# Kernel tuning notes

Measured on AMD Instinct MI355X. Metric: run time of the kernel, lower is better.

## Reference

```python
import jax, jax.numpy as jnp
import numpy as np

B, T, CIN, CH, M, NCLS = 2048, 8, 2048, 1024, 32, 21
EPS = 1e-8  # torch.cosine_similarity eps


def setup_inputs() -> dict:
    key = jax.random.key(0)
    ks = jax.random.split(key, 16)
    g = lambda k, shp, sc=0.02: jax.random.normal(k, shp, dtype=jnp.float32) * sc
    return {
        "x": g(ks[0], (B, T, CIN), 1.0),
        "static_feat": g(ks[1], (NCLS, CIN, M), 1.0),  # 21 kmeans exemplar banks
        "Wk": g(ks[2], (CH, CIN)), "bk": g(ks[3], (CH,)),
        "Wv": g(ks[4], (CH, CIN)), "bv": g(ks[5], (CH,)),
        "WEk": g(ks[6], (CH, CIN)), "bEk": g(ks[7], (CH,)),
        "WEv": g(ks[8], (CH, CIN)), "bEv": g(ks[9], (CH,)),
        "Ww": g(ks[10], (1, CH)), "bw": g(ks[11], (1,)),
        "Wout": g(ks[12], (NCLS, 2 * CH)), "bout": g(ks[13], (NCLS,)),
    }


def reference(x, static_feat, Wk, bk, Wv, bv, WEk, bEk, WEv, bEv, Ww, bw, Wout, bout):
    # last frame only: [B, CIN]
    xl = x[:, -1, :]
    # 1x1 convs on length-1 sequence == dense projections
    k = xl @ Wk.T + bk          # [B, CH]
    v = xl @ Wv.T + bv          # [B, CH]
    # project all 21 static memories at once: [NCLS, CH, M]
    Ek = jnp.einsum('oc,ncm->nom', WEk, static_feat) + bEk[None, :, None]
    Ev = jnp.einsum('oc,ncm->nom', WEv, static_feat) + bEv[None, :, None]
    # cosine similarity along channel dim (torch clamps each norm at eps)
    kn = k / jnp.maximum(jnp.linalg.norm(k, axis=1, keepdims=True), EPS)
    Ekn = Ek / jnp.maximum(jnp.linalg.norm(Ek, axis=1, keepdims=True), EPS)
    cos = jnp.einsum('bo,nom->bnm', kn, Ekn)      # [B, NCLS, M]
    w = jax.nn.softmax(cos, axis=-1)               # softmax over exemplars
    s = jnp.einsum('nom,bnm->bno', Ev, w)          # weighted sums [B, NCLS, CH]
    # per-class scalar weights via conv2_1_W, softmax over the 21 classes
    fw = jax.nn.softmax(s @ Ww[0] + bw[0], axis=-1)  # [B, NCLS]
    fE = jnp.einsum('bno,bn->bo', s, fw)             # [B, CH]
    h = jax.nn.relu(jnp.concatenate([v, fE], axis=-1))  # [B, 2*CH]
    out = h @ Wout.T + bout                              # [B, NCLS]
    return out[:, :, None]  # [B, NCLS, 1] to match Conv1d output
```

## Files before the change

### kernel.cpp

```cpp
#include <hip/hip_runtime.h>
#include <math.h>

#define B_    2048
#define T_    8
#define CIN_  2048
#define CH_   1024
#define M_    32
#define NCLS_ 21
#define NM_   (NCLS_*M_)
#define NMP_  768
#define EPS_  1e-8f
#define ZKV_  2
#define ZC_   2

typedef __bf16 bf16_t;
typedef bf16_t bf16x4 __attribute__((ext_vector_type(4)));
typedef bf16_t bf16x8 __attribute__((ext_vector_type(8)));
typedef float  floatx4 __attribute__((ext_vector_type(4)));

#define GLOBAL_AS __attribute__((address_space(1)))
#define LDS_AS    __attribute__((address_space(3)))

__global__ __launch_bounds__(256) void gemm128(
    const bf16_t* __restrict__ A0, const bf16_t* __restrict__ A1, int msplit,
    const bf16_t* __restrict__ B0, const bf16_t* __restrict__ B1,
    const float* __restrict__ bias0, const float* __restrict__ bias1,
    int ld, bf16_t* __restrict__ C, int ldc, size_t strideC, int mzero, int Ksplit)
{
  __shared__ bf16_t As[128 * 64];
  __shared__ bf16_t Bs[128 * 64];
  const int tid = threadIdx.x;
  const int n0 = blockIdx.x * 128, m0 = blockIdx.y * 128;
  const int z = blockIdx.z;

  const bf16_t* A; const bf16_t* B; const float* bias; int mrow;
  if (m0 < msplit) { A = A0; B = B0; bias = bias0; mrow = m0; }
  else             { A = A1; B = B1; bias = bias1; mrow = m0 - msplit; }
  const int koff = z * Ksplit;

  const int w = tid >> 6, lane = tid & 63;
  const int srow = lane >> 3;
  const int sblk = (lane & 7) ^ srow;
  const bf16_t* ga = A + (size_t)(mrow + w * 32 + srow) * ld + koff + sblk * 8;
  const bf16_t* gb = B + (size_t)(n0   + w * 32 + srow) * ld + koff + sblk * 8;

  const int wm = (w >> 1) * 64, wn = (w & 1) * 64;
  const int l15 = lane & 15, quad = lane >> 4;
  const int sx = l15 & 7;

  floatx4 acc[4][4] = {};

  for (int k0 = 0; k0 < Ksplit; k0 += 64) {
    __syncthreads();
    #pragma unroll
    for (int q = 0; q < 4; ++q) {
      __builtin_amdgcn_global_load_lds(
          (const GLOBAL_AS void*)(ga + (size_t)q * 8 * ld),
          (LDS_AS void*)(&As[(w * 4 + q) * 512]), 16, 0, 0);
      __builtin_amdgcn_global_load_lds(
          (const GLOBAL_AS void*)(gb + (size_t)q * 8 * ld),
          (LDS_AS void*)(&Bs[(w * 4 + q) * 512]), 16, 0, 0);
    }
    ga += 64; gb += 64;
    __syncthreads();
    #pragma unroll
    for (int ks = 0; ks < 2; ++ks) {
      bf16x8 af[4], bfr[4];
      #pragma unroll
      for (int i = 0; i < 4; ++i)
        af[i] = *(const bf16x8*)(&As[(wm + i * 16 + l15) * 64 + ((ks * 4 + quad) ^ sx) * 8]);
      #pragma unroll
      for (int j = 0; j < 4; ++j)
        bfr[j] = *(const bf16x8*)(&Bs[(wn + j * 16 + l15) * 64 + ((ks * 4 + quad) ^ sx) * 8]);
      #pragma unroll
      for (int i = 0; i < 4; ++i)
        #pragma unroll
        for (int j = 0; j < 4; ++j)
          acc[i][j] = __builtin_amdgcn_mfma_f32_16x16x32_bf16(af[i], bfr[j], acc[i][j], 0, 0, 0);
    }
  }

  bf16_t* Cz = C + (size_t)z * strideC;
  #pragma unroll
  for (int i = 0; i < 4; ++i) {
    const int rbase = m0 + wm + i * 16 + quad * 4;
    #pragma unroll
    for (int j = 0; j < 4; ++j) {
      const int c = n0 + wn + j * 16 + l15;
      const float badd = (bias && z == 0) ? bias[c] : 0.f;
      #pragma unroll
      for (int r = 0; r < 4; ++r) {
        const int rr = rbase + r;
        float v = acc[i][j][r] + badd;
        if (rr >= mzero) v = 0.f;
        Cz[(size_t)rr * ldc + c] = (bf16_t)v;
      }
    }
  }
}

template<int MODE>
__global__ __launch_bounds__(256) void gemm_n64(
    const bf16_t* __restrict__ A, const bf16_t* __restrict__ B, int ld,
    bf16_t* __restrict__ Cb, int ldc, size_t strideC, int Ksplit)
{
  __shared__ bf16_t As[128 * 64];
  __shared__ bf16_t Bs[64 * 64];
  const int tid = threadIdx.x;
  const int n0 = blockIdx.x * 64, m0 = blockIdx.y * 128;
  const int z = blockIdx.z;
  const int koff = z * Ksplit;

  const int w = tid >> 6, lane = tid & 63;
  const int srow = lane >> 3;
  const int sblk = (lane & 7) ^ srow;
  const bf16_t* ga = A + (size_t)(m0 + w * 32 + srow) * ld + koff + sblk * 8;
  const bf16_t* gb = B + (size_t)(n0 + w * 16 + srow) * ld + koff + sblk * 8;

  const int l15 = lane & 15, quad = lane >> 4;
  const int sx = l15 & 7;

  floatx4 acc[2][4] = {};

  for (int k0 = 0; k0 < Ksplit; k0 += 64) {
    __syncthreads();
    #pragma unroll
    for (int q = 0; q < 4; ++q)
      __builtin_amdgcn_global_load_lds(
          (const GLOBAL_AS void*)(ga + (size_t)q * 8 * ld),
          (LDS_AS void*)(&As[(w * 4 + q) * 512]), 16, 0, 0);
    #pragma unroll
    for (int q = 0; q < 2; ++q)
      __builtin_amdgcn_global_load_lds(
          (const GLOBAL_AS void*)(gb + (size_t)q * 8 * ld),
          (LDS_AS void*)(&Bs[(w * 2 + q) * 512]), 16, 0, 0);
    ga += 64; gb += 64;
    __syncthreads();
    #pragma unroll
    for (int ks = 0; ks < 2; ++ks) {
      bf16x8 af[2], bfr[4];
      #pragma unroll
      for (int i = 0; i < 2; ++i)
        af[i] = *(const bf16x8*)(&As[(w * 32 + i * 16 + l15) * 64 + ((ks * 4 + quad) ^ sx) * 8]);
      #pragma unroll
      for (int j = 0; j < 4; ++j)
        bfr[j] = *(const bf16x8*)(&Bs[(j * 16 + l15) * 64 + ((ks * 4 + quad) ^ sx) * 8]);
      #pragma unroll
      for (int i = 0; i < 2; ++i)
        #pragma unroll
        for (int j = 0; j < 4; ++j)
          acc[i][j] = __builtin_amdgcn_mfma_f32_16x16x32_bf16(af[i], bfr[j], acc[i][j], 0, 0, 0);
    }
  }

  bf16_t* Cz = Cb + (size_t)z * strideC;
  #pragma unroll
  for (int i = 0; i < 2; ++i) {
    const int rbase = m0 + w * 32 + i * 16 + quad * 4;
    #pragma unroll
    for (int j = 0; j < 4; ++j) {
      const int c = n0 + j * 16 + l15;
      #pragma unroll
      for (int r = 0; r < 4; ++r) {
        const int rr = rbase + r;
        const float v = acc[i][j][r];
        Cz[(size_t)rr * ldc + c] = (bf16_t)(MODE == 1 ? fmaxf(v, 0.f) : v);
      }
    }
  }
}

__global__ __launch_bounds__(256) void kPrepAll(
    const float* __restrict__ x, const float* __restrict__ Wk,
    const float* __restrict__ Wv, const float* __restrict__ WEk,
    const float* __restrict__ WEv, const float* __restrict__ bk,
    const float* __restrict__ bv, const float* __restrict__ bEk,
    const float* __restrict__ bEv, const float* __restrict__ Wout,
    const float* __restrict__ sf,
    bf16_t* __restrict__ xb, bf16_t* __restrict__ Wkvb, bf16_t* __restrict__ WEb,
    bf16_t* __restrict__ Woutb, bf16_t* __restrict__ sfTb,
    float* __restrict__ bkv, float* __restrict__ bE)
{
  __shared__ float t[32][33];
  const int blk = blockIdx.x;
  const int tid = threadIdx.x;

  if (blk >= 3084) {
    const int tt = blk - 3084;
    const int nn = tt % 24;
    const int c0 = (tt / 24) * 32;
    const int cc = tid & 31, r8 = tid >> 5;
    #pragma unroll
    for (int q = 0; q < 4; ++q) {
      const int cl = r8 + q * 8;
      float v = 0.f;
      if (nn < NCLS_) v = sf[((size_t)nn * CIN_ + c0 + cl) * M_ + cc];
      t[cl][cc] = v;
    }
    __syncthreads();
    #pragma unroll
    for (int q = 0; q < 4; ++q) {
      const int ml = r8 + q * 8;
      sfTb[(size_t)(nn * 32 + ml) * CIN_ + c0 + cc] = (bf16_t)t[cc][ml];
    }
    return;
  }
  if (blk == 3072) {
    for (int i = tid; i < CH_; i += 256) {
      bkv[i] = bk[i]; bkv[CH_ + i] = bv[i];
      bE[i]  = bEk[i]; bE[CH_ + i] = bEv[i];
    }
    return;
  }
  if (blk > 3072) {
    const size_t e0 = ((size_t)(blk - 3073) * 256 + tid) * 16;
    if (e0 < (size_t)NCLS_ * 2 * CH_) {
      #pragma unroll
      for (int q = 0; q < 4; ++q) {
        const float4 v = *(const float4*)(Wout + e0 + q * 4);
        bf16x4 o = { (bf16_t)v.x, (bf16_t)v.y, (bf16_t)v.z, (bf16_t)v.w };
        *(bf16x4*)(Woutb + e0 + q * 4) = o;
      }
    }
    return;
  }
  const int sec = blk >> 10;
  const int tt = ((blk & 1023) << 8) + tid;
  const size_t e0 = (size_t)tt * 16;
  const int row = (int)(e0 >> 11);
  const int col = (int)(e0 & 2047);
  const float* src;
  bf16_t* dst;
  if (sec == 0) {
    src = x + (size_t)row * (T_ * CIN_) + (size_t)(T_ - 1) * CIN_ + col;
    dst = xb + e0;
  } else if (sec == 1) {
    src = (row < CH_ ? Wk + (size_t)row * CIN_ : Wv + (size_t)(row - CH_) * CIN_) + col;
    dst = Wkvb + e0;
  } else {
    src = (row < CH_ ? WEk + (size_t)row * CIN_ : WEv + (size_t)(row - CH_) * CIN_) + col;
    dst = WEb + e0;
  }
  #pragma unroll
  for (int q = 0; q < 4; ++q) {
    const float4 v = *(const float4*)(src + q * 4);
    bf16x4 o = { (bf16_t)v.x, (bf16_t)v.y, (bf16_t)v.z, (bf16_t)v.w };
    *(bf16x4*)(dst + q * 4) = o;
  }
}

__global__ __launch_bounds__(256) void kNormTr(
    const bf16_t* __restrict__ KVE, size_t PS, const float* __restrict__ Ww,
    bf16_t* __restrict__ knb, bf16_t* __restrict__ Eknb, float* __restrict__ EvW,
    bf16_t* __restrict__ Ev2b)
{
  __shared__ float t[32][33];
  const int blk = blockIdx.x;
  const int tid = threadIdx.x;

  if (blk < 704) {
    const int r = blk * 4 + (tid >> 6);
    const int lane = tid & 63;
    const bf16_t* row = KVE + (size_t)r * 2048;
    float vals[16];
    float ss = 0.f;
    #pragma unroll
    for (int i = 0; i < 16; ++i) {
      const int o = lane + i * 64;
      float v = (float)row[o];
      #pragma unroll
      for (int z = 1; z < ZKV_; ++z) v += (float)row[(size_t)z * PS + o];
      vals[i] = v;
      ss += v * v;
    }
    for (int off = 32; off; off >>= 1) ss += __shfl_xor(ss, off);
    const float inv = 1.f / fmaxf(sqrtf(ss), EPS_);
    bf16_t* dst = (r < B_) ? knb + (size_t)r * CH_ : Eknb + (size_t)(r - B_) * CH_;
    #pragma unroll
    for (int i = 0; i < 16; ++i) dst[lane + i * 64] = (bf16_t)(vals[i] * inv);
    if (r >= B_) {
      float dd = 0.f;
      for (int o = lane; o < CH_; o += 64) {
        float v = (float)row[CH_ + o];
        #pragma unroll
        for (int z = 1; z < ZKV_; ++z) v += (float)row[(size_t)z * PS + CH_ + o];
        dd += v * Ww[o];
      }
      for (int off = 32; off; off >>= 1) dd += __shfl_xor(dd, off);
      if (lane == 0) EvW[r - B_] = dd;
    }
    return;
  }
  const int tt = blk - 704;
  const int nm0 = (tt % 24) * 32;
  const int o0 = (tt / 24) * 32;
  const int cc = tid & 31, r8 = tid >> 5;
  #pragma unroll
  for (int q = 0; q < 4; ++q) {
    const int r = r8 + q * 8;
    const size_t idx = (size_t)(B_ + nm0 + r) * 2048 + CH_ + o0 + cc;
    float v = (float)KVE[idx];
    #pragma unroll
    for (int z = 1; z < ZKV_; ++z) v += (float)KVE[(size_t)z * PS + idx];
    t[r][cc] = v;
  }
  __syncthreads();
  #pragma unroll
  for (int q = 0; q < 4; ++q) {
    const int r = r8 + q * 8;
    Ev2b[(size_t)(o0 + r) * NMP_ + nm0 + cc] = (bf16_t)t[cc][r];
  }
}

__global__ __launch_bounds__(256) void kSoftmax(
    const bf16_t* __restrict__ cosb, size_t PSc,
    const float* __restrict__ EvW, const float* __restrict__ bw,
    bf16_t* __restrict__ wwb)
{
  const int b = blockIdx.x;
  const int tid = threadIdx.x;
  __shared__ float sc[NM_];
  __shared__ float sl[NCLS_];
  for (int i = tid; i < NM_; i += 256) {
    float v = (float)cosb[(size_t)b * NMP_ + i];
    #pragma unroll
    for (int z = 1; z < ZC_; ++z) v += (float)cosb[(size_t)z * PSc + (size_t)b * NMP_ + i];
    sc[i] = v;
  }
  __syncthreads();
  if (tid < NCLS_) {
    const int base = tid * M_;
    float mx = -1e30f;
    for (int m = 0; m < M_; ++m) mx = fmaxf(mx, sc[base + m]);
    float s = 0.f;
    for (int m = 0; m < M_; ++m) {
      const float e = __expf(sc[base + m] - mx);
      sc[base + m] = e;
      s += e;
    }
    const float inv = 1.f / s;
    float lg = 0.f;
    for (int m = 0; m < M_; ++m) {
      const float w = sc[base + m] * inv;
      sc[base + m] = w;
      lg += w * EvW[base + m];
    }
    sl[tid] = lg + bw[0];
  }
  __syncthreads();
  if (tid == 0) {
    float mx = -1e30f;
    for (int n = 0; n < NCLS_; ++n) mx = fmaxf(mx, sl[n]);
    float s = 0.f;
    for (int n = 0; n < NCLS_; ++n) { const float e = __expf(sl[n] - mx); sl[n] = e; s += e; }
    const float inv = 1.f / s;
    for (int n = 0; n < NCLS_; ++n) sl[n] *= inv;
  }
  __syncthreads();
  for (int i = tid; i < NMP_; i += 256) {
    const float v = (i < NM_) ? sc[i] * sl[i >> 5] : 0.f;
    wwb[(size_t)b * NMP_ + i] = (bf16_t)v;
  }
}

__global__ __launch_bounds__(256) void kOut(
    const bf16_t* __restrict__ KVE, size_t PS,
    const bf16_t* __restrict__ fEb, const bf16_t* __restrict__ Woutb,
    const float* __restrict__ bout, float* __restrict__ out)
{
  const int b = blockIdx.x;
  const int tid = threadIdx.x;
  __shared__ float h[2 * CH_];
  for (int j = tid; j < CH_; j += 256) {
    const size_t idx = (size_t)b * 2048 + CH_ + j;
    float v = (float)KVE[idx];
    #pragma unroll
    for (int z = 1; z < ZKV_; ++z) v += (float)KVE[(size_t)z * PS + idx];
    h[j] = fmaxf(v, 0.f);
  }
  for (int j = tid; j < CH_; j += 256)
    h[CH_ + j] = (float)fEb[(size_t)b * CH_ + j];
  __syncthreads();
  const int wave = tid >> 6, lane = tid & 63;
  for (int n = wave; n < NCLS_; n += 4) {
    const bf16_t* wr = Woutb + (size_t)n * (2 * CH_);
    float s = 0.f;
    for (int j = lane; j < 2 * CH_; j += 64) s += h[j] * (float)wr[j];
    for (int off = 32; off; off >>= 1) s += __shfl_xor(s, off);
    if (lane == 0) out[(size_t)b * NCLS_ + n] = s + bout[n];
  }
}

extern "C" void kernel_launch(void* const* d_in, const int* in_sizes, int n_in,
                              void* d_out, int out_size, void* d_ws, size_t ws_size,
                              hipStream_t stream)
{
  const float* x    = (const float*)d_in[0];
  const float* sf   = (const float*)d_in[1];
  const float* Wk   = (const float*)d_in[2];
  const float* bk   = (const float*)d_in[3];
  const float* Wv   = (const float*)d_in[4];
  const float* bv   = (const float*)d_in[5];
  const float* WEk  = (const float*)d_in[6];
  const float* bEk  = (const float*)d_in[7];
  const float* WEv  = (const float*)d_in[8];
  const float* bEv  = (const float*)d_in[9];
  const float* Ww   = (const float*)d_in[10];
  const float* bw   = (const float*)d_in[11];
  const float* Wout = (const float*)d_in[12];
  const float* bout = (const float*)d_in[13];
  float* out = (float*)d_out;

  char* ws = (char*)d_ws;
  size_t off = 0;
  auto alloc = [&](size_t bytes) { char* p = ws + off; off += (bytes + 255) & ~(size_t)255; return p; };
  const size_t PS  = (size_t)2816 * 2048;
  const size_t PSc = (size_t)B_ * NMP_;
  bf16_t* KVE   = (bf16_t*)alloc(PS * ZKV_ * 2);
  bf16_t* xb    = (bf16_t*)alloc((size_t)2048 * 2048 * 2);
  bf16_t* Wkvb  = (bf16_t*)alloc((size_t)2048 * 2048 * 2);
  bf16_t* WEb   = (bf16_t*)alloc((size_t)2048 * 2048 * 2);
  bf16_t* sfTb  = (bf16_t*)alloc((size_t)NMP_ * 2048 * 2);
  bf16_t* knb   = (bf16_t*)alloc((size_t)B_ * CH_ * 2);
  bf16_t* Eknb  = (bf16_t*)alloc((size_t)NMP_ * CH_ * 2);
  bf16_t* Ev2b  = (bf16_t*)alloc((size_t)CH_ * NMP_ * 2);
  bf16_t* cosb  = (bf16_t*)alloc(PSc * ZC_ * 2);
  bf16_t* wwb   = (bf16_t*)alloc((size_t)B_ * NMP_ * 2);
  bf16_t* fEb   = (bf16_t*)alloc((size_t)B_ * CH_ * 2);
  bf16_t* Woutb = (bf16_t*)alloc((size_t)NCLS_ * 2 * CH_ * 2);
  float*  bkv   = (float*)alloc(2 * CH_ * 4);
  float*  bE    = (float*)alloc(2 * CH_ * 4);
  float*  EvW   = (float*)alloc(NMP_ * 4);

  kPrepAll<<<4620, 256, 0, stream>>>(x, Wk, Wv, WEk, WEv, bk, bv, bEk, bEv,
                                     Wout, sf, xb, Wkvb, WEb, Woutb, sfTb,
                                     bkv, bE);
  gemm128<<<dim3(16, 22, ZKV_), 256, 0, stream>>>(
      xb, sfTb, B_, Wkvb, WEb, bkv, bE, CIN_,
      KVE, 2048, PS, B_ + NM_, CIN_ / ZKV_);
  kNormTr<<<1472, 256, 0, stream>>>(KVE, PS, Ww, knb, Eknb, EvW, Ev2b);
  gemm_n64<0><<<dim3(NMP_ / 64, 16, ZC_), 256, 0, stream>>>(
      knb, Eknb, CH_, cosb, NMP_, PSc, CH_ / ZC_);
  kSoftmax<<<B_, 256, 0, stream>>>(cosb, PSc, EvW, bw, wwb);
  gemm_n64<1><<<dim3(CH_ / 64, 16, 1), 256, 0, stream>>>(
      wwb, Ev2b, NMP_, fEb, CH_, 0, NMP_);
  kOut<<<B_, 256, 0, stream>>>(KVE, PS, fEb, Woutb, bout, out);
}
```

Baseline: 349.3 us.

## Build concatenated relu hidden buffer upstream and batch 8 rows per output block

The relu(v) half of the hidden vector is now computed in the normalization kernel and written as bf16 into a shared [B,2048] buffer. The fE GEMM writes directly into the second half of that buffer with a row stride of 2048. The output kernel then loads 8 batch rows into LDS with vectorized loads and reuses each Wout vector load across those rows. This cuts the split-K re-reads and the per-row weight traffic in the final projection, at the cost of rounding v to bf16 and using more LDS per block.

```diff
diff --git a/kernel.cpp b/kernel.cpp
--- a/kernel.cpp
+++ b/kernel.cpp
@@ -252,7 +252,7 @@
 __global__ __launch_bounds__(256) void kNormTr(
     const bf16_t* __restrict__ KVE, size_t PS, const float* __restrict__ Ww,
     bf16_t* __restrict__ knb, bf16_t* __restrict__ Eknb, float* __restrict__ EvW,
-    bf16_t* __restrict__ Ev2b)
+    bf16_t* __restrict__ Ev2b, bf16_t* __restrict__ hb)
 {
   __shared__ float t[32][33];
   const int blk = blockIdx.x;
@@ -278,7 +278,16 @@
     bf16_t* dst = (r < B_) ? knb + (size_t)r * CH_ : Eknb + (size_t)(r - B_) * CH_;
     #pragma unroll
     for (int i = 0; i < 16; ++i) dst[lane + i * 64] = (bf16_t)(vals[i] * inv);
-    if (r >= B_) {
+    if (r < B_) {
+      #pragma unroll
+      for (int i = 0; i < 16; ++i) {
+        const int o = CH_ + lane + i * 64;
+        float v = (float)row[o];
+        #pragma unroll
+        for (int z = 1; z < ZKV_; ++z) v += (float)row[(size_t)z * PS + o];
+        hb[(size_t)r * 2048 + lane + i * 64] = (bf16_t)fmaxf(v, 0.f);
+      }
+    } else {
       float dd = 0.f;
       for (int o = lane; o < CH_; o += 64) {
         float v = (float)row[CH_ + o];
@@ -363,31 +372,44 @@
   }
 }
 
-__global__ __launch_bounds__(256) void kOut(
-    const bf16_t* __restrict__ KVE, size_t PS,
-    const bf16_t* __restrict__ fEb, const bf16_t* __restrict__ Woutb,
+__global__ __launch_bounds__(256) void kOutW(
+    const bf16_t* __restrict__ hb, const bf16_t* __restrict__ Woutb,
     const float* __restrict__ bout, float* __restrict__ out)
 {
-  const int b = blockIdx.x;
-  const int tid = threadIdx.x;
-  __shared__ float h[2 * CH_];
-  for (int j = tid; j < CH_; j += 256) {
-    const size_t idx = (size_t)b * 2048 + CH_ + j;
-    float v = (float)KVE[idx];
-    #pragma unroll
-    for (int z = 1; z < ZKV_; ++z) v += (float)KVE[(size_t)z * PS + idx];
-    h[j] = fmaxf(v, 0.f);
-  }
-  for (int j = tid; j < CH_; j += 256)
-    h[CH_ + j] = (float)fEb[(size_t)b * CH_ + j];
+  __shared__ bf16_t hs[8][2048];
+  const int b0 = blockIdx.x * 8;
+  const int tid = threadIdx.x;
+  #pragma unroll
+  for (int q = 0; q < 8; ++q) {
+    const int idx = q * 256 + tid;
+    const int row = idx >> 8;
+    const int col = (idx & 255) * 8;
+    *(bf16x8*)&hs[row][col] = *(const bf16x8*)&hb[(size_t)(b0 + row) * 2048 + col];
+  }
   __syncthreads();
-  const int wave = tid >> 6, lane = tid & 63;
-  for (int n = wave; n < NCLS_; n += 4) {
-    const bf16_t* wr = Woutb + (size_t)n * (2 * CH_);
-    float s = 0.f;
-    for (int j = lane; j < 2 * CH_; j += 64) s += h[j] * (float)wr[j];
-    for (int off = 32; off; off >>= 1) s += __shfl_xor(s, off);
-    if (lane == 0) out[(size_t)b * NCLS_ + n] = s + bout[n];
+  const int w = tid >> 6, lane = tid & 63;
+  for (int n = w; n < NCLS_; n += 4) {
+    const bf16_t* wr = Woutb + (size_t)n * 2048;
+    float a[8] = {};
+    #pragma unroll
+    for (int q = 0; q < 4; ++q) {
+      const int k0 = q * 512 + lane * 8;
+      const bf16x8 wv = *(const bf16x8*)&wr[k0];
+      #pragma unroll
+      for (int r = 0; r < 8; ++r) {
+        const bf16x8 hv = *(const bf16x8*)&hs[r][k0];
+        float s = 0.f;
+        #pragma unroll
+        for (int e = 0; e < 8; ++e) s += (float)hv[e] * (float)wv[e];
+        a[r] += s;
+      }
+    }
+    #pragma unroll
+    for (int r = 0; r < 8; ++r) {
+      float s = a[r];
+      for (int off = 32; off; off >>= 1) s += __shfl_xor(s, off);
+      if (lane == 0) out[(size_t)(b0 + r) * NCLS_ + n] = s + bout[n];
+    }
   }
 }
 
@@ -426,7 +448,7 @@
   bf16_t* Ev2b  = (bf16_t*)alloc((size_t)CH_ * NMP_ * 2);
   bf16_t* cosb  = (bf16_t*)alloc(PSc * ZC_ * 2);
   bf16_t* wwb   = (bf16_t*)alloc((size_t)B_ * NMP_ * 2);
-  bf16_t* fEb   = (bf16_t*)alloc((size_t)B_ * CH_ * 2);
+  bf16_t* hb    = (bf16_t*)alloc((size_t)B_ * 2048 * 2);
   bf16_t* Woutb = (bf16_t*)alloc((size_t)NCLS_ * 2 * CH_ * 2);
   float*  bkv   = (float*)alloc(2 * CH_ * 4);
   float*  bE    = (float*)alloc(2 * CH_ * 4);
@@ -438,11 +460,11 @@
   gemm128<<<dim3(16, 22, ZKV_), 256, 0, stream>>>(
       xb, sfTb, B_, Wkvb, WEb, bkv, bE, CIN_,
       KVE, 2048, PS, B_ + NM_, CIN_ / ZKV_);
-  kNormTr<<<1472, 256, 0, stream>>>(KVE, PS, Ww, knb, Eknb, EvW, Ev2b);
+  kNormTr<<<1472, 256, 0, stream>>>(KVE, PS, Ww, knb, Eknb, EvW, Ev2b, hb);
   gemm_n64<0><<<dim3(NMP_ / 64, 16, ZC_), 256, 0, stream>>>(
       knb, Eknb, CH_, cosb, NMP_, PSc, CH_ / ZC_);
   kSoftmax<<<B_, 256, 0, stream>>>(cosb, PSc, EvW, bw, wwb);
   gemm_n64<1><<<dim3(CH_ / 64, 16, 1), 256, 0, stream>>>(
-      wwb, Ev2b, NMP_, fEb, CH_, 0, NMP_);
-  kOut<<<B_, 256, 0, stream>>>(KVE, PS, fEb, Woutb, bout, out);
-}
+      wwb, Ev2b, NMP_, hb + CH_, 2048, 0, NMP_);
+  kOutW<<<B_ / 8, 256, 0, stream>>>(hb, Woutb, bout, out);
+}
```

Measured after the change: 314.3 us (median of 2 runs). 1.11x faster.
